# Performance work log

Hardware: AMD Instinct MI355X
Metric: run time of the kernel (lower is better)

## Reference

```python
import jax, jax.numpy as jnp
import numpy as np

N = 50000      # total nodes
NPG = 1000     # nodes per graph
B = 50         # graphs in batch
E = 800000     # positive edges
HID = 64
LN_EPS = 1e-5


def setup_inputs() -> dict:
    key = jax.random.key(0)
    ks = jax.random.split(key, 8)
    h = jax.random.normal(ks[0], (N, HID), jnp.float32)
    W1 = jax.random.normal(ks[1], (HID + 1, 2 * HID), jnp.float32) * 0.1
    b1 = jnp.zeros((2 * HID,), jnp.float32)
    ln_g = jnp.ones((2 * HID,), jnp.float32)
    ln_b = jnp.zeros((2 * HID,), jnp.float32)
    W2 = jax.random.normal(ks[2], (2 * HID, 1), jnp.float32) * 0.1
    b2 = jnp.zeros((1,), jnp.float32)
    # positive edges: endpoints within the same graph (contiguous node blocks)
    src_p = jax.random.randint(ks[3], (E,), 0, N)
    dst_p = (src_p // NPG) * NPG + jax.random.randint(ks[4], (E,), 0, NPG)
    pos_edge = jnp.stack([src_p, dst_p]).astype(jnp.int32)
    # negative edges: same-graph random pairs (stand-in for batched_negative_sampling)
    src_n = jax.random.randint(ks[5], (E,), 0, N)
    dst_n = (src_n // NPG) * NPG + jax.random.randint(ks[6], (E,), 0, NPG)
    neg_edge = jnp.stack([src_n, dst_n]).astype(jnp.int32)
    node_batch = jnp.arange(N, dtype=jnp.int32) // NPG
    return {"h": h, "W1": W1, "b1": b1, "ln_g": ln_g, "ln_b": ln_b,
            "W2": W2, "b2": b2, "pos_edge": pos_edge, "neg_edge": neg_edge,
            "node_batch": node_batch, "num_graphs": B}


def reference(h, W1, b1, ln_g, ln_b, W2, b2, pos_edge, neg_edge, node_batch, num_graphs):
    Epos = pos_edge.shape[1]
    T = 2 * Epos
    nb = int(num_graphs)
    # concat pos+neg edges, stable sort by graph id of source node
    edges_all = jnp.concatenate([pos_edge, neg_edge], axis=1)      # [2, T]
    idx = jnp.argsort(node_batch[edges_all[0]])                    # stable
    edges = edges_all[:, idx]
    conn = (idx < Epos).astype(h.dtype)                            # 1 = positive edge
    # pair features + connectivity flag -> tiny MLP score
    enc = jnp.concatenate([h[edges[0]] + h[edges[1]], conn[:, None]], axis=-1)  # [T, HID+1]
    x = enc @ W1 + b1                                              # [T, 2*HID]
    mu = jnp.mean(x, axis=-1, keepdims=True)
    var = jnp.mean((x - mu) ** 2, axis=-1, keepdims=True)
    x = (x - mu) * jax.lax.rsqrt(var + LN_EPS) * ln_g + ln_b
    x = jax.nn.relu(x)
    logits = (x @ W2)[:, 0] + b2[0]                                # [T]
    # ragged per-graph top-k: k = floor(0.9 * pos-degree count per graph)
    seg = node_batch[edges[0]]                                     # sorted segment ids
    k = jnp.floor(jax.ops.segment_sum(jnp.ones((Epos,), jnp.float32),
                                      node_batch[pos_edge[0]], num_segments=nb) * 0.9).astype(jnp.int32)
    counts = jax.ops.segment_sum(jnp.ones((T,), jnp.int32), seg, num_segments=nb)
    starts = jnp.cumsum(counts) - counts                           # segment offsets
    perm = jnp.lexsort((-logits, seg))                             # within-segment desc by logit
    seg_p = seg[perm]
    pos_in_seg = jnp.arange(T, dtype=jnp.int32) - starts[seg_p]
    mask = jnp.zeros((T,), bool).at[perm].set(pos_in_seg < k[seg_p])
    edge_weight = jnp.where(mask, logits, jnp.zeros((), logits.dtype))
    # node mask: nodes touched by any selected edge
    node_idx = edges.reshape(-1)
    vals = jnp.concatenate([mask, mask]).astype(jnp.int32)
    node_mask = jnp.zeros((h.shape[0],), jnp.int32).at[node_idx].add(vals) > 0
    return mask, edge_weight, node_mask
```

## Files before the change

### kernel.cpp

```cpp
#include <hip/hip_runtime.h>
#include <cstdint>

typedef unsigned long long u64;
typedef unsigned int u32;
typedef float f2 __attribute__((ext_vector_type(2)));

#define NGRAPH  50
#define EPOS    800000
#define TEDGE   1600000
#define HID     64
#define D2      128
#define CHUNK   1024
#define NCHUNK  1563
#define HSTRIDE 1564
#define LN_EPS  1e-5f
#define CANDCAP 4096
#define HPBLK   782

__device__ __forceinline__ f2 mkf2(float a, float b) { f2 r; r.x = a; r.y = b; return r; }

__device__ __forceinline__ int seg_of(int node) { return (int)((u32)node / 1000u); }

__device__ __forceinline__ u32 mapkey32(float f) {
    u32 u = __float_as_uint(f);
    return (u >> 31) ? ~u : (u | 0x80000000u);
}
__device__ __forceinline__ float unmapkey32(u32 k) {
    u32 u = (k & 0x80000000u) ? (k & 0x7FFFFFFFu) : ~k;
    return __uint_as_float(u);
}

__device__ __forceinline__ float red8(float x) {
    int t = __builtin_amdgcn_mov_dpp(__float_as_int(x), 0xB1, 0xF, 0xF, true);
    x += __int_as_float(t);
    t = __builtin_amdgcn_mov_dpp(__float_as_int(x), 0x4E, 0xF, 0xF, true);
    x += __int_as_float(t);
    t = __builtin_amdgcn_ds_swizzle(__float_as_int(x), 0x101F);
    x += __int_as_float(t);
    return x;
}

template <int NBITS>
__device__ __forceinline__ void agg_add(u32* hist, bool act, u32 bin, int lane) {
    u64 peers = __ballot(act);
#pragma unroll
    for (int b = 0; b < NBITS; ++b) {
        bool bit = (bin >> b) & 1;
        u64 bb = __ballot(act && bit);
        peers &= bit ? bb : ~bb;
    }
    if (act && (peers & ((1ull << lane) - 1ull)) == 0)
        atomicAdd(&hist[bin], (u32)__popcll(peers));
}

__device__ __forceinline__ void suffix_select(const u32* histL, u32 r, u32* wsumL,
                                              u32* selBin, u32* selRem,
                                              int tid, int lane, int wv) {
    u32 h0 = histL[2 * tid], h1 = histL[2 * tid + 1];
    u32 chunk = h0 + h1;
    u32 inc = chunk;
#pragma unroll
    for (int d = 1; d < 64; d <<= 1) {
        u32 t = __shfl_down(inc, d);
        if (lane + d < 64) inc += t;
    }
    if (lane == 0) wsumL[wv] = inc;
    __syncthreads();
    u32 S = inc;
    for (int w = wv + 1; w < 16; ++w) S += wsumL[w];
    u32 sufExcl = S - chunk;
    u32 incl1 = sufExcl + h1, incl0 = incl1 + h0;
    if (sufExcl < r && r <= incl1) { *selBin = 2 * tid + 1; *selRem = r - sufExcl; }
    else if (incl1 < r && r <= incl0) { *selBin = 2 * tid; *selRem = r - incl1; }
    __syncthreads();
}

__global__ __launch_bounds__(256) void hp_hist_kernel(const float* __restrict__ h,
                                                      const float* __restrict__ W1,
                                                      const float* __restrict__ b1,
                                                      float* __restrict__ hp,
                                                      const int* __restrict__ pos,
                                                      const int* __restrict__ neg,
                                                      int* __restrict__ histAll,
                                                      int* __restrict__ histPos) {
    __shared__ float w1s[HID * D2];
    __shared__ float hs[64 * 65];
    __shared__ int hA[NGRAPH], hP[NGRAPH];
    int bid = blockIdx.x, tid = threadIdx.x, lane = tid & 63;

    if (bid < HPBLK) {
        int n0 = bid * 64;
        for (int t = tid; t < HID * D2 / 4; t += 256)
            ((float4*)w1s)[t] = ((const float4*)W1)[t];
        for (int t = tid; t < 4096; t += 256) {
            int n = t >> 6, k = t & 63;
            int node = n0 + n;
            hs[n * 65 + k] = (node < 50000) ? h[node * HID + k] : 0.0f;
        }
        __syncthreads();
        int cg = tid & 15, ng = tid >> 4;
        int jc = cg * 8, nn = ng * 4;
        double acc[4][8];
#pragma unroll
        for (int n = 0; n < 4; ++n)
#pragma unroll
            for (int j = 0; j < 8; ++j) acc[n][j] = 0.0;
        for (int k = 0; k < HID; ++k) {
            float hv[4];
#pragma unroll
            for (int n = 0; n < 4; ++n) hv[n] = hs[(nn + n) * 65 + k];
            float4 w0 = *(const float4*)&w1s[k * D2 + jc];
            float4 w1v = *(const float4*)&w1s[k * D2 + jc + 4];
            float wf[8] = {w0.x, w0.y, w0.z, w0.w, w1v.x, w1v.y, w1v.z, w1v.w};
#pragma unroll
            for (int n = 0; n < 4; ++n)
#pragma unroll
                for (int j = 0; j < 8; ++j)
                    acc[n][j] += (double)hv[n] * (double)wf[j];
        }
        double bh[8];
#pragma unroll
        for (int j = 0; j < 8; ++j) bh[j] = 0.5 * (double)b1[jc + j];
#pragma unroll
        for (int n = 0; n < 4; ++n) {
            int node = n0 + nn + n;
            if (node < 50000) {
                float4 o0 = make_float4((float)(acc[n][0] + bh[0]), (float)(acc[n][1] + bh[1]),
                                        (float)(acc[n][2] + bh[2]), (float)(acc[n][3] + bh[3]));
                float4 o1 = make_float4((float)(acc[n][4] + bh[4]), (float)(acc[n][5] + bh[5]),
                                        (float)(acc[n][6] + bh[6]), (float)(acc[n][7] + bh[7]));
                *(float4*)&hp[node * D2 + jc] = o0;
                *(float4*)&hp[node * D2 + jc + 4] = o1;
            }
        }
    } else {
        int c = bid - HPBLK;
        if (tid < NGRAPH) { hA[tid] = 0; hP[tid] = 0; }
        __syncthreads();
        int base = c * CHUNK;
#pragma unroll
        for (int r = 0; r < 4; ++r) {
            int e = base + r * 256 + tid;
            bool valid = e < TEDGE;
            int seg = 0; bool isPos = false;
            if (valid) {
                int src = (e < EPOS) ? pos[e] : neg[e - EPOS];
                seg = seg_of(src);
                isPos = e < EPOS;
            }
            u64 peers = __ballot(valid);
#pragma unroll
            for (int b = 0; b < 6; ++b) {
                bool bit = (seg >> b) & 1;
                u64 bb = __ballot(bit);
                peers &= bit ? bb : ~bb;
            }
            u64 bpos = __ballot(isPos);
            u64 low = (1ull << lane) - 1ull;
            if (valid) {
                if ((peers & low) == 0) atomicAdd(&hA[seg], __popcll(peers));
                u64 pp = peers & bpos;
                if (isPos && (pp & low) == 0) atomicAdd(&hP[seg], __popcll(pp));
            }
        }
        __syncthreads();
        if (tid < NGRAPH) {
            histAll[tid * HSTRIDE + c] = hA[tid];
            histPos[tid * HSTRIDE + c] = hP[tid];
        }
    }
}

__global__ __launch_bounds__(1024) void scan_kernel(const int* __restrict__ histAll,
                                                    const int* __restrict__ histPos,
                                                    int* __restrict__ chunkBase,
                                                    int* __restrict__ segStart,
                                                    int* __restrict__ segCnt,
                                                    int* __restrict__ kArr,
                                                    float* __restrict__ outNm) {
    __shared__ int totA[NGRAPH], totP[NGRAPH], segStartL[NGRAPH];
    int g = blockIdx.x, tid = threadIdx.x, lane = tid & 63, wv = tid >> 6;

    if (tid < 1000) outNm[g * 1000 + tid] = 0.0f;

    for (int s = wv; s < NGRAPH; s += 16) {
        int ta = 0, tp = 0;
        for (int c = lane; c < NCHUNK; c += 64) {
            ta += histAll[s * HSTRIDE + c];
            tp += histPos[s * HSTRIDE + c];
        }
        for (int m = 32; m >= 1; m >>= 1) {
            ta += __shfl_xor(ta, m);
            tp += __shfl_xor(tp, m);
        }
        if (lane == 0) { totA[s] = ta; totP[s] = tp; }
    }
    __syncthreads();
    if (tid == 0) {
        int run = 0;
        for (int s = 0; s < NGRAPH; ++s) {
            segStartL[s] = run;
            if (g == 0) {
                segStart[s] = run;
                segCnt[s] = totA[s];
                kArr[s] = (int)floorf((float)totP[s] * 0.9f);
            }
            run += totA[s];
        }
    }
    __syncthreads();
    if (wv == 0) {
        int run = segStartL[g];
        for (int b0 = 0; b0 < NCHUNK; b0 += 64) {
            int c = b0 + lane;
            int v = (c < NCHUNK) ? histAll[g * HSTRIDE + c] : 0;
            int inc = v;
            for (int d = 1; d < 64; d <<= 1) {
                int t = __shfl_up(inc, d);
                if (lane >= d) inc += t;
            }
            if (c < NCHUNK) chunkBase[g * HSTRIDE + c] = run + (inc - v);
            run += __shfl(inc, 63);
        }
    }
}

__global__ __launch_bounds__(256) void scatter_kernel(const int* __restrict__ pos,
                                                      const int* __restrict__ neg,
                                                      const int* __restrict__ chunkBase,
                                                      int2* __restrict__ sortedE,
                                                      u32* __restrict__ selHist) {
    __shared__ int cbL[52];
    __shared__ int wcnL[4][52];
    int c = blockIdx.x, tid = threadIdx.x, lane = tid & 63, wv = tid >> 6;
    if (c < 400) selHist[c * 256 + tid] = 0u;
    if (tid < NGRAPH) cbL[tid] = chunkBase[tid * HSTRIDE + c];
    int base = c * CHUNK;
#pragma unroll
    for (int r = 0; r < 4; ++r) {
        if (tid < 4 * 52) ((int*)wcnL)[tid] = 0;
        __syncthreads();
        int e = base + r * 256 + tid;
        bool valid = e < TEDGE;
        int seg = 0, src = 0, dst = 0, flag = 0;
        if (valid) {
            if (e < EPOS) { src = pos[e]; dst = pos[EPOS + e]; flag = 1 << 30; }
            else          { src = neg[e - EPOS]; dst = neg[e]; flag = 0; }
            seg = seg_of(src);
        }
        u64 peers = __ballot(valid);
#pragma unroll
        for (int b = 0; b < 6; ++b) {
            bool bit = (seg >> b) & 1;
            u64 bb = __ballot(bit);
            peers &= bit ? bb : ~bb;
        }
        int intra = 0;
        if (valid) {
            u64 low = (1ull << lane) - 1ull;
            intra = __popcll(peers & low);
            if ((peers & low) == 0) wcnL[wv][seg] = __popcll(peers);
        }
        __syncthreads();
        if (tid < NGRAPH) {
            int run = cbL[tid];
#pragma unroll
            for (int w = 0; w < 4; ++w) {
                int cc = wcnL[w][tid];
                wcnL[w][tid] = run;
                run += cc;
            }
            cbL[tid] = run;
        }
        __syncthreads();
        if (valid) sortedE[wcnL[wv][seg] + intra] = make_int2(src | flag, dst);
        __syncthreads();
    }
}

#define LG_BLOCKS 6400
__global__ __launch_bounds__(256, 4) void logits_kernel(const float* __restrict__ hp,
                                                        const float* __restrict__ W1,
                                                        const float* __restrict__ lng,
                                                        const float* __restrict__ lnb,
                                                        const float* __restrict__ W2,
                                                        const float* __restrict__ b2,
                                                        const int2* __restrict__ sortedE,
                                                        u32* __restrict__ keysU) {
    int tid = threadIdx.x, wv = tid >> 6, lane = tid & 63;
    int grp = lane >> 3, q = lane & 7;
    int xcd = blockIdx.x & 7;
    int wg = (blockIdx.x >> 3) * 4 + wv;
    int edge0 = (xcd * 3200 + wg) * 64;
    if (edge0 >= TEDGE) return;

    const float4* hp4 = (const float4*)hp;
    const float4* W1r = (const float4*)(W1 + HID * D2);
    f2 wv2[8], gv2[8], ev2[8], vv2[8];
#pragma unroll
    for (int a = 0; a < 4; ++a) {
        float4 w4 = W1r[q + 8 * a];
        float4 g4 = ((const float4*)lng)[q + 8 * a];
        float4 e4 = ((const float4*)lnb)[q + 8 * a];
        float4 v4 = ((const float4*)W2)[q + 8 * a];
        wv2[2*a] = mkf2(w4.x, w4.y); wv2[2*a+1] = mkf2(w4.z, w4.w);
        gv2[2*a] = mkf2(g4.x, g4.y); gv2[2*a+1] = mkf2(g4.z, g4.w);
        ev2[2*a] = mkf2(e4.x, e4.y); ev2[2*a+1] = mkf2(e4.z, e4.w);
        vv2[2*a] = mkf2(v4.x, v4.y); vv2[2*a+1] = mkf2(v4.z, v4.w);
    }
    float bias2 = b2[0];

    int e0 = edge0 + grp;
    int2 edA = sortedE[e0];
    int2 edB = sortedE[e0 + 8];
    float4 A[4], D[4];
    {
        int src = edA.x & 0x3FFFFFFF, dst = edA.y;
#pragma unroll
        for (int a = 0; a < 4; ++a) {
            A[a] = hp4[src * 32 + q + 8 * a];
            D[a] = hp4[dst * 32 + q + 8 * a];
        }
    }

#pragma unroll
    for (int it = 0; it < 8; ++it) {
        int ecur = edge0 + it * 8 + grp;
        float connf = (float)((edA.x >> 30) & 1);
        f2 conn2 = mkf2(connf, connf);

        f2 xv[8];
#pragma unroll
        for (int a = 0; a < 4; ++a) {
            f2 alo = mkf2(A[a].x, A[a].y) + mkf2(D[a].x, D[a].y);
            f2 ahi = mkf2(A[a].z, A[a].w) + mkf2(D[a].z, D[a].w);
            xv[2*a]   = __builtin_elementwise_fma(conn2, wv2[2*a],   alo);
            xv[2*a+1] = __builtin_elementwise_fma(conn2, wv2[2*a+1], ahi);
        }

        if (it < 7) {
            int srcB = edB.x & 0x3FFFFFFF, dstB = edB.y;
#pragma unroll
            for (int a = 0; a < 4; ++a) {
                A[a] = hp4[srcB * 32 + q + 8 * a];
                D[a] = hp4[dstB * 32 + q + 8 * a];
            }
            edA = edB;
            if (it < 6) edB = sortedE[edge0 + (it + 2) * 8 + grp];
        }

        f2 s01 = xv[0] + xv[1], s23 = xv[2] + xv[3];
        f2 s45 = xv[4] + xv[5], s67 = xv[6] + xv[7];
        f2 sT = (s01 + s23) + (s45 + s67);
        f2 q0 = xv[0] * xv[0], q1 = xv[1] * xv[1], q2 = xv[2] * xv[2], q3 = xv[3] * xv[3];
        f2 q4 = xv[4] * xv[4], q5 = xv[5] * xv[5], q6 = xv[6] * xv[6], q7 = xv[7] * xv[7];
        f2 qT = ((q0 + q1) + (q2 + q3)) + ((q4 + q5) + (q6 + q7));
        float s = red8(sT.x + sT.y);
        float s2 = red8(qT.x + qT.y);
        float mu = s * 0.0078125f;
        float var = fmaf(s2, 0.0078125f, -(mu * mu)) + LN_EPS;
        float rinv = 1.0f / sqrtf(var);
        float mc = -mu * rinv;
        f2 rinv2 = mkf2(rinv, rinv), mc2 = mkf2(mc, mc), zero2 = mkf2(0.f, 0.f);

        f2 zacc = zero2;
#pragma unroll
        for (int kk = 0; kk < 8; ++kk) {
            f2 t = __builtin_elementwise_fma(xv[kk], rinv2, mc2);
            t = __builtin_elementwise_fma(t, gv2[kk], ev2[kk]);
            f2 y = __builtin_elementwise_max(t, zero2);
            zacc = __builtin_elementwise_fma(y, vv2[kk], zacc);
        }
        float z = red8(zacc.x + zacc.y);
        if (q == 0) keysU[ecur] = mapkey32(z + bias2);
    }
}

__global__ __launch_bounds__(256) void selhist_kernel(const u32* __restrict__ keysU,
                                                      const int* __restrict__ segStart,
                                                      const int* __restrict__ segCnt,
                                                      const int* __restrict__ kArr,
                                                      u32* __restrict__ selHist) {
    __shared__ u32 hb[2048];
    int bid = blockIdx.x, tid = threadIdx.x, lane = tid & 63;
    int seg = bid >> 3, slice = bid & 7;
    int start = segStart[seg], cnt = segCnt[seg], k = kArr[seg];
    if (k <= 0 || k >= cnt) return;
#pragma unroll
    for (int b = 0; b < 8; ++b) hb[tid + 256 * b] = 0u;
    __syncthreads();
    int i0 = start + (int)((long long)cnt * slice / 8);
    int i1 = start + (int)((long long)cnt * (slice + 1) / 8);
    int n = i1 - i0, iters = (n + 255) >> 8;
    for (int j = 0; j < iters; ++j) {
        int i = j * 256 + tid;
        bool act = i < n;
        u32 key = act ? keysU[i0 + i] : 0u;
        agg_add<11>(hb, act, key >> 21, lane);
    }
    __syncthreads();
#pragma unroll
    for (int b = 0; b < 8; ++b) {
        u32 v = hb[tid + 256 * b];
        if (v) atomicAdd(&selHist[seg * 2048 + tid + 256 * b], v);
    }
}

__global__ __launch_bounds__(1024) void segout_kernel(const u32* __restrict__ keysU,
                                                      const int2* __restrict__ sortedE,
                                                      const int* __restrict__ segStart,
                                                      const int* __restrict__ segCnt,
                                                      const int* __restrict__ kArr,
                                                      const u32* __restrict__ selHist,
                                                      float* __restrict__ outMask,
                                                      float* __restrict__ outEw,
                                                      float* __restrict__ outNm) {
    __shared__ u64 arr[CANDCAP];
    __shared__ int candN;
    __shared__ u32 histL[2048];
    __shared__ u32 wsumL[16];
    __shared__ u32 selBin, selRem;
    __shared__ int tieCnt;
    __shared__ int tieIdx[1024];
    int g = blockIdx.x, tid = threadIdx.x, lane = tid & 63, wv = tid >> 6;
    int start = segStart[g], cnt = segCnt[g], k = kArr[g];
    if (tid == 0) { candN = 0; tieCnt = 0; }

    u32 B; int r;
    if (k <= 0)        { B = 0xFFFFFFFFu; r = 0;  __syncthreads(); }
    else if (k >= cnt) { B = 0xFFFFFFFFu; r = -1; __syncthreads(); }
    else {
        histL[tid] = selHist[g * 2048 + tid];
        histL[tid + 1024] = selHist[g * 2048 + 1024 + tid];
        __syncthreads();
        suffix_select(histL, (u32)k, wsumL, &selBin, &selRem, tid, lane, wv);
        B = selBin; r = (int)selRem;
    }

    int iters = (cnt + 1023) >> 10;
    for (int j = 0; j < iters; ++j) {
        int i = j * 1024 + tid;
        if (i < cnt) {
            int idx = start + i;
            u32 key = keysU[idx];
            u32 pre = key >> 21;
            bool gt = (r < 0) || (pre > B);
            outMask[idx] = gt ? 1.0f : 0.0f;
            outEw[idx] = gt ? unmapkey32(key) : 0.0f;
            if (gt) {
                int2 ed = sortedE[idx];
                outNm[ed.x & 0x3FFFFFFF] = 1.0f;
                outNm[ed.y] = 1.0f;
            } else if (r > 0 && pre == B) {
                int p = atomicAdd(&candN, 1);
                if (p < CANDCAP) arr[p] = ((u64)(~key) << 32) | (u32)idx;
            }
        }
    }
    __syncthreads();
    if (r <= 0) return;
    int nc = candN;

    if (nc <= CANDCAP) {
        int N = 64;
        while (N < nc) N <<= 1;
        for (int t = tid; t < N; t += 1024)
            if (t >= nc) arr[t] = ~0ull;
        __syncthreads();
        for (int kk = 2; kk <= N; kk <<= 1) {
            for (int j = kk >> 1; j > 0; j >>= 1) {
                for (int i = tid; i < N; i += 1024) {
                    int l = i ^ j;
                    if (l > i) {
                        u64 a = arr[i], b = arr[l];
                        bool up = ((i & kk) == 0);
                        if ((a > b) == up) { arr[i] = b; arr[l] = a; }
                    }
                }
                __syncthreads();
            }
        }
        for (int t = tid; t < r && t < nc; t += 1024) {
            u64 v = arr[t];
            int idx = (int)(u32)v;
            u32 key = ~(u32)(v >> 32);
            outMask[idx] = 1.0f;
            outEw[idx] = unmapkey32(key);
            int2 ed = sortedE[idx];
            outNm[ed.x & 0x3FFFFFFF] = 1.0f;
            outNm[ed.y] = 1.0f;
        }
    } else {
        histL[tid] = 0; histL[tid + 1024] = 0;
        __syncthreads();
        for (int j = 0; j < iters; ++j) {
            int i = j * 1024 + tid;
            bool act = i < cnt;
            u32 key = act ? keysU[start + i] : 0u;
            act = act && ((key >> 21) == B);
            agg_add<11>(histL, act, (key >> 10) & 0x7FFu, lane);
        }
        __syncthreads();
        suffix_select(histL, (u32)r, wsumL, &selBin, &selRem, tid, lane, wv);
        u32 pref2 = (B << 11) | selBin;
        u32 r2 = selRem;
        histL[tid] = 0; histL[tid + 1024] = 0;
        __syncthreads();
        for (int j = 0; j < iters; ++j) {
            int i = j * 1024 + tid;
            bool act = i < cnt;
            u32 key = act ? keysU[start + i] : 0u;
            act = act && ((key >> 10) == pref2);
            agg_add<10>(histL, act, key & 0x3FFu, lane);
        }
        __syncthreads();
        suffix_select(histL, r2, wsumL, &selBin, &selRem, tid, lane, wv);
        u32 vKey = (pref2 << 10) | selBin;
        int m = (int)selRem;
        for (int j = 0; j < iters; ++j) {
            int i = j * 1024 + tid;
            if (i < cnt) {
                int idx = start + i;
                u32 key = keysU[idx];
                if ((key >> 21) == B) {
                    if (key > vKey) {
                        outMask[idx] = 1.0f;
                        outEw[idx] = unmapkey32(key);
                        int2 ed = sortedE[idx];
                        outNm[ed.x & 0x3FFFFFFF] = 1.0f;
                        outNm[ed.y] = 1.0f;
                    } else if (key == vKey) {
                        int t = atomicAdd(&tieCnt, 1);
                        if (t < 1024) tieIdx[t] = idx;
                    }
                }
            }
        }
        __syncthreads();
        if (wv == 0 && m > 0) {
            int t = tieCnt < 1024 ? tieCnt : 1024;
            float vLg = unmapkey32(vKey);
            for (int b0 = 0; b0 < t; b0 += 64) {
                int mine = (b0 + lane < t) ? tieIdx[b0 + lane] : 0x7FFFFFFF;
                int rank = 0;
                for (int j = 0; j < t; ++j)
                    rank += (tieIdx[j] < mine) ? 1 : 0;
                if (b0 + lane < t && rank < m) {
                    outMask[mine] = 1.0f;
                    outEw[mine] = vLg;
                    int2 ed = sortedE[mine];
                    outNm[ed.x & 0x3FFFFFFF] = 1.0f;
                    outNm[ed.y] = 1.0f;
                }
            }
        }
    }
}

extern "C" void kernel_launch(void* const* d_in, const int* in_sizes, int n_in,
                              void* d_out, int out_size, void* d_ws, size_t ws_size,
                              hipStream_t stream) {
    const float* h   = (const float*)d_in[0];
    const float* W1  = (const float*)d_in[1];
    const float* b1  = (const float*)d_in[2];
    const float* lng = (const float*)d_in[3];
    const float* lnb = (const float*)d_in[4];
    const float* W2  = (const float*)d_in[5];
    const float* b2  = (const float*)d_in[6];
    const int* pos   = (const int*)d_in[7];
    const int* neg   = (const int*)d_in[8];

    char* ws = (char*)d_ws;
    float*  hp          = (float*)(ws + 0);
    int2*   sortedE     = (int2*)(ws + 25600000);
    u32*    keysU       = (u32*)(ws + 38400000);
    int*    histAll     = (int*)(ws + 44800000);
    int*    histPos     = (int*)(ws + 45112800);
    int*    chunkBase   = (int*)(ws + 45425600);
    u32*    selHist     = (u32*)(ws + 44800000);
    int*    segStart    = (int*)(ws + 45738400);
    int*    segCnt      = (int*)(ws + 45738656);
    int*    kArr        = (int*)(ws + 45738912);

    float* outF    = (float*)d_out;
    float* outMask = outF;
    float* outEw   = outF + TEDGE;
    float* outNm   = outF + 2 * TEDGE;

    hipLaunchKernelGGL(hp_hist_kernel, dim3(HPBLK + NCHUNK), dim3(256), 0, stream,
                       h, W1, b1, hp, pos, neg, histAll, histPos);
    hipLaunchKernelGGL(scan_kernel, dim3(NGRAPH), dim3(1024), 0, stream,
                       histAll, histPos, chunkBase, segStart, segCnt, kArr, outNm);
    hipLaunchKernelGGL(scatter_kernel, dim3(NCHUNK), dim3(256), 0, stream,
                       pos, neg, chunkBase, sortedE, selHist);
    hipLaunchKernelGGL(logits_kernel, dim3(LG_BLOCKS), dim3(256), 0, stream,
                       hp, W1, lng, lnb, W2, b2, sortedE, keysU);
    hipLaunchKernelGGL(selhist_kernel, dim3(400), dim3(256), 0, stream,
                       keysU, segStart, segCnt, kArr, selHist);
    hipLaunchKernelGGL(segout_kernel, dim3(NGRAPH), dim3(1024), 0, stream,
                       keysU, sortedE, segStart, segCnt, kArr, selHist,
                       outMask, outEw, outNm);
}
```

Baseline: 336.4 us.

## Split per-segment output pass into bin-find, wide sweep, and final tie-resolve kernels

The single 50-block segout kernel is split into three kernels. One finds the threshold bin per segment, one sweeps all edges with 1600 blocks writing mask, weight and node-mask outputs while appending boundary candidates to a global buffer through wave-aggregated atomics, and a final per-segment kernel sorts those candidates. This spreads the memory-bound sweep across the whole GPU instead of 50 workgroups. The cost is two extra launches, plus global candidate traffic in place of LDS, with candBuf reusing the hp workspace region.

```diff
diff --git a/kernel.cpp b/kernel.cpp
--- a/kernel.cpp
+++ b/kernel.cpp
@@ -16,6 +16,7 @@
 #define LN_EPS  1e-5f
 #define CANDCAP 4096
 #define HPBLK   782
+#define SWSLICE 32
 
 __device__ __forceinline__ f2 mkf2(float a, float b) { f2 r; r.x = a; r.y = b; return r; }
 
@@ -406,62 +407,105 @@
     }
 }
 
-__global__ __launch_bounds__(1024) void segout_kernel(const u32* __restrict__ keysU,
-                                                      const int2* __restrict__ sortedE,
-                                                      const int* __restrict__ segStart,
-                                                      const int* __restrict__ segCnt,
-                                                      const int* __restrict__ kArr,
-                                                      const u32* __restrict__ selHist,
-                                                      float* __restrict__ outMask,
-                                                      float* __restrict__ outEw,
-                                                      float* __restrict__ outNm) {
+__global__ __launch_bounds__(1024) void binfind_kernel(const int* __restrict__ segCnt,
+                                                       const int* __restrict__ kArr,
+                                                       const u32* __restrict__ selHist,
+                                                       int* __restrict__ selB,
+                                                       int* __restrict__ selR,
+                                                       u32* __restrict__ candCnt) {
+    __shared__ u32 histL[2048];
+    __shared__ u32 wsumL[16];
+    __shared__ u32 selBin, selRem;
+    int g = blockIdx.x, tid = threadIdx.x, lane = tid & 63, wv = tid >> 6;
+    int cnt = segCnt[g], k = kArr[g];
+    u32 B; int r;
+    if (k <= 0)        { B = 0xFFFFFFFFu; r = 0; }
+    else if (k >= cnt) { B = 0xFFFFFFFFu; r = -1; }
+    else {
+        histL[tid] = selHist[g * 2048 + tid];
+        histL[tid + 1024] = selHist[g * 2048 + 1024 + tid];
+        __syncthreads();
+        suffix_select(histL, (u32)k, wsumL, &selBin, &selRem, tid, lane, wv);
+        B = selBin; r = (int)selRem;
+    }
+    if (tid == 0) { selB[g] = (int)B; selR[g] = r; candCnt[g] = 0u; }
+}
+
+__global__ __launch_bounds__(256) void segsweep_kernel(const u32* __restrict__ keysU,
+                                                       const int2* __restrict__ sortedE,
+                                                       const int* __restrict__ segStart,
+                                                       const int* __restrict__ segCnt,
+                                                       const int* __restrict__ selB,
+                                                       const int* __restrict__ selR,
+                                                       u32* __restrict__ candCnt,
+                                                       u64* __restrict__ candBuf,
+                                                       float* __restrict__ outMask,
+                                                       float* __restrict__ outEw,
+                                                       float* __restrict__ outNm) {
+    int bid = blockIdx.x, tid = threadIdx.x, lane = tid & 63;
+    int g = bid / SWSLICE, slice = bid % SWSLICE;
+    int start = segStart[g], cnt = segCnt[g];
+    u32 B = (u32)selB[g]; int r = selR[g];
+    int i0 = (int)((long long)cnt * slice / SWSLICE);
+    int i1 = (int)((long long)cnt * (slice + 1) / SWSLICE);
+    int n = i1 - i0, iters = (n + 255) >> 8;
+    bool wantCand = (r > 0);
+    for (int j = 0; j < iters; ++j) {
+        int i = i0 + j * 256 + tid;
+        bool act = i < i1;
+        int idx = start + i;
+        u32 key = act ? keysU[idx] : 0u;
+        u32 pre = key >> 21;
+        bool gt = act && ((r < 0) || (pre > B));
+        if (act) {
+            outMask[idx] = gt ? 1.0f : 0.0f;
+            outEw[idx] = gt ? unmapkey32(key) : 0.0f;
+            if (gt) {
+                int2 ed = sortedE[idx];
+                outNm[ed.x & 0x3FFFFFFF] = 1.0f;
+                outNm[ed.y] = 1.0f;
+            }
+        }
+        bool cand = act && wantCand && !gt && (pre == B);
+        u64 bmask = __ballot(cand);
+        if (cand) {
+            int firstl = (int)(__ffsll((unsigned long long)bmask) - 1);
+            u32 base = 0;
+            if (lane == firstl) base = atomicAdd(&candCnt[g], (u32)__popcll(bmask));
+            base = __shfl(base, firstl);
+            u32 p = base + (u32)__popcll(bmask & ((1ull << lane) - 1ull));
+            if (p < CANDCAP) candBuf[g * CANDCAP + p] = ((u64)(~key) << 32) | (u32)idx;
+        }
+    }
+}
+
+__global__ __launch_bounds__(1024) void segfinal_kernel(const u32* __restrict__ keysU,
+                                                        const int2* __restrict__ sortedE,
+                                                        const int* __restrict__ segStart,
+                                                        const int* __restrict__ segCnt,
+                                                        const int* __restrict__ selB,
+                                                        const int* __restrict__ selR,
+                                                        const u32* __restrict__ candCnt,
+                                                        const u64* __restrict__ candBuf,
+                                                        float* __restrict__ outMask,
+                                                        float* __restrict__ outEw,
+                                                        float* __restrict__ outNm) {
     __shared__ u64 arr[CANDCAP];
-    __shared__ int candN;
     __shared__ u32 histL[2048];
     __shared__ u32 wsumL[16];
     __shared__ u32 selBin, selRem;
     __shared__ int tieCnt;
     __shared__ int tieIdx[1024];
     int g = blockIdx.x, tid = threadIdx.x, lane = tid & 63, wv = tid >> 6;
-    int start = segStart[g], cnt = segCnt[g], k = kArr[g];
-    if (tid == 0) { candN = 0; tieCnt = 0; }
-
-    u32 B; int r;
-    if (k <= 0)        { B = 0xFFFFFFFFu; r = 0;  __syncthreads(); }
-    else if (k >= cnt) { B = 0xFFFFFFFFu; r = -1; __syncthreads(); }
-    else {
-        histL[tid] = selHist[g * 2048 + tid];
-        histL[tid + 1024] = selHist[g * 2048 + 1024 + tid];
-        __syncthreads();
-        suffix_select(histL, (u32)k, wsumL, &selBin, &selRem, tid, lane, wv);
-        B = selBin; r = (int)selRem;
-    }
-
-    int iters = (cnt + 1023) >> 10;
-    for (int j = 0; j < iters; ++j) {
-        int i = j * 1024 + tid;
-        if (i < cnt) {
-            int idx = start + i;
-            u32 key = keysU[idx];
-            u32 pre = key >> 21;
-            bool gt = (r < 0) || (pre > B);
-            outMask[idx] = gt ? 1.0f : 0.0f;
-            outEw[idx] = gt ? unmapkey32(key) : 0.0f;
-            if (gt) {
-                int2 ed = sortedE[idx];
-                outNm[ed.x & 0x3FFFFFFF] = 1.0f;
-                outNm[ed.y] = 1.0f;
-            } else if (r > 0 && pre == B) {
-                int p = atomicAdd(&candN, 1);
-                if (p < CANDCAP) arr[p] = ((u64)(~key) << 32) | (u32)idx;
-            }
-        }
-    }
+    int start = segStart[g], cnt = segCnt[g];
+    u32 B = (u32)selB[g]; int r = selR[g];
+    if (r <= 0) return;
+    int nc = (int)candCnt[g];
+    if (tid == 0) tieCnt = 0;
     __syncthreads();
-    if (r <= 0) return;
-    int nc = candN;
 
     if (nc <= CANDCAP) {
+        for (int t = tid; t < nc; t += 1024) arr[t] = candBuf[g * CANDCAP + t];
         int N = 64;
         while (N < nc) N <<= 1;
         for (int t = tid; t < N; t += 1024)
@@ -491,6 +535,7 @@
             outNm[ed.y] = 1.0f;
         }
     } else {
+        int iters = (cnt + 1023) >> 10;
         histL[tid] = 0; histL[tid + 1024] = 0;
         __syncthreads();
         for (int j = 0; j < iters; ++j) {
@@ -581,6 +626,10 @@
     int*    segStart    = (int*)(ws + 45738400);
     int*    segCnt      = (int*)(ws + 45738656);
     int*    kArr        = (int*)(ws + 45738912);
+    u32*    candCnt     = (u32*)(ws + 0);
+    int*    selB        = (int*)(ws + 1024);
+    int*    selR        = (int*)(ws + 2048);
+    u64*    candBuf     = (u64*)(ws + 8192);
 
     float* outF    = (float*)d_out;
     float* outMask = outF;
@@ -597,7 +646,12 @@
                        hp, W1, lng, lnb, W2, b2, sortedE, keysU);
     hipLaunchKernelGGL(selhist_kernel, dim3(400), dim3(256), 0, stream,
                        keysU, segStart, segCnt, kArr, selHist);
-    hipLaunchKernelGGL(segout_kernel, dim3(NGRAPH), dim3(1024), 0, stream,
-                       keysU, sortedE, segStart, segCnt, kArr, selHist,
-                       outMask, outEw, outNm);
-}
+    hipLaunchKernelGGL(binfind_kernel, dim3(NGRAPH), dim3(1024), 0, stream,
+                       segCnt, kArr, selHist, selB, selR, candCnt);
+    hipLaunchKernelGGL(segsweep_kernel, dim3(NGRAPH * SWSLICE), dim3(256), 0, stream,
+                       keysU, sortedE, segStart, segCnt, selB, selR,
+                       candCnt, candBuf, outMask, outEw, outNm);
+    hipLaunchKernelGGL(segfinal_kernel, dim3(NGRAPH), dim3(1024), 0, stream,
+                       keysU, sortedE, segStart, segCnt, selB, selR,
+                       candCnt, candBuf, outMask, outEw, outNm);
+}
```

Result: slower. 465.7 us (+38.5%).
